# Kernel optimization log

Hardware: AMD Instinct MI355X
Metric: run time of the kernel (lower is better)

Reference implementation:

```python
import jax, jax.numpy as jnp
import numpy as np
from jax import lax

B, T, H, IN = 2048, 2048, 25, 1


def setup_inputs() -> dict:
    key = jax.random.key(0)
    ks = jax.random.split(key, 7)
    s = 1.0 / np.sqrt(H)  # PyTorch LSTM init scale
    return {
        "x": jax.random.normal(ks[0], (B, T, IN), dtype=jnp.float32),
        "w_ih": jax.random.uniform(ks[1], (4 * H, IN), jnp.float32, -s, s),
        "w_hh": jax.random.uniform(ks[2], (4 * H, H), jnp.float32, -s, s),
        "b_ih": jax.random.uniform(ks[3], (4 * H,), jnp.float32, -s, s),
        "b_hh": jax.random.uniform(ks[4], (4 * H,), jnp.float32, -s, s),
        "w_dense": jax.random.uniform(ks[5], (1, H), jnp.float32, -s, s),
        "b_dense": jax.random.uniform(ks[6], (1,), jnp.float32, -s, s),
    }


def reference(x, w_ih, w_hh, b_ih, b_hh, w_dense, b_dense):
    # x: [B, T, 1] -> scan over time on [T, B, *]
    xt = jnp.swapaxes(x, 0, 1)                     # [T, B, IN]
    x_proj = xt @ w_ih.T + (b_ih + b_hh)           # [T, B, 4H], input projection precomputed

    def step(carry, xp):
        h, c = carry
        gates = xp + h @ w_hh.T                    # [B, 4H]
        i, f, g, o = jnp.split(gates, 4, axis=-1)  # PyTorch gate order i,f,g,o
        i = jax.nn.sigmoid(i)
        f = jax.nn.sigmoid(f)
        g = jnp.tanh(g)
        o = jax.nn.sigmoid(o)
        c = f * c + i * g
        h = o * jnp.tanh(c)
        return (h, c), h

    h0 = jnp.zeros((x.shape[0], H), dtype=x.dtype)
    c0 = jnp.zeros((x.shape[0], H), dtype=x.dtype)
    _, hs = lax.scan(step, (h0, c0), x_proj)       # hs: [T, B, H]
    hs = jnp.swapaxes(hs, 0, 1)                    # [B, T, H]
    return hs @ w_dense.T + b_dense                # [B, T, 1]
```

## Files before the change

kernel.cpp:

```cpp
#include <hip/hip_runtime.h>

#define T_LEN 2048
#define HID   25
#define LOG2E 1.4426950408889634f

typedef float vf4 __attribute__((vector_size(16), may_alias));
typedef float vf2 __attribute__((vector_size(8),  may_alias));
typedef float f2  __attribute__((ext_vector_type(2)));

__device__ __forceinline__ float fast_rcp(float x) { return __builtin_amdgcn_rcpf(x); }
__device__ __forceinline__ float fast_exp2(float x) { return __builtin_amdgcn_exp2f(x); }


__global__ __attribute__((amdgpu_flat_work_group_size(256, 256),
                          amdgpu_waves_per_eu(1, 1)))
void lstm_fused(
    const float* __restrict__ x,
    const float* __restrict__ w_ih,
    const float* __restrict__ w_hh,
    const float* __restrict__ b_ih,
    const float* __restrict__ b_hh,
    const float* __restrict__ w_dense,
    const float* __restrict__ b_dense,
    float* __restrict__ out)
{
    const int tid  = threadIdx.x;
    const int u    = tid & 31;
    const int cb   = tid >> 5;
    const int b    = blockIdx.x * 8 + cb;
    const bool act = u < HID;

    __shared__ __align__(16) float hbuf[16][32];

    const float si = -LOG2E, sg = 2.f * LOG2E;

    f2 wI2[13], wF2[13], wG2[13], wO2[13];
#pragma unroll
    for (int m = 0; m < 12; ++m) {
        wI2[m] = act ? f2{si * w_hh[u * HID + m],             si * w_hh[u * HID + m + 12]}             : f2{0.f, 0.f};
        wF2[m] = act ? f2{si * w_hh[(HID + u) * HID + m],     si * w_hh[(HID + u) * HID + m + 12]}     : f2{0.f, 0.f};
        wG2[m] = act ? f2{sg * w_hh[(2 * HID + u) * HID + m], sg * w_hh[(2 * HID + u) * HID + m + 12]} : f2{0.f, 0.f};
        wO2[m] = act ? f2{si * w_hh[(3 * HID + u) * HID + m], si * w_hh[(3 * HID + u) * HID + m + 12]} : f2{0.f, 0.f};
    }
    wI2[12] = act ? f2{si * w_hh[u * HID + 24], 0.f}             : f2{0.f, 0.f};
    wF2[12] = act ? f2{si * w_hh[(HID + u) * HID + 24], 0.f}     : f2{0.f, 0.f};
    wG2[12] = act ? f2{sg * w_hh[(2 * HID + u) * HID + 24], 0.f} : f2{0.f, 0.f};
    wO2[12] = act ? f2{si * w_hh[(3 * HID + u) * HID + 24], 0.f} : f2{0.f, 0.f};

    const float bI  = act ? si * (b_ih[u] + b_hh[u]) : 0.f;
    const float bF  = act ? si * (b_ih[HID + u] + b_hh[HID + u]) : 0.f;
    const float bG  = act ? sg * (b_ih[2 * HID + u] + b_hh[2 * HID + u]) : 0.f;
    const float bO  = act ? si * (b_ih[3 * HID + u] + b_hh[3 * HID + u]) : 0.f;
    const float wxI = act ? si * w_ih[u] : 0.f;
    const float wxF = act ? si * w_ih[HID + u] : 0.f;
    const float wxG = act ? sg * w_ih[2 * HID + u] : 0.f;
    const float wxO = act ? si * w_ih[3 * HID + u] : 0.f;
    const float bd  = b_dense[0];

    f2 wd2[13];
#pragma unroll
    for (int m = 0; m < 12; ++m) wd2[m] = f2{w_dense[m], w_dense[m + 12]};
    wd2[12] = f2{w_dense[24], 0.f};

    hbuf[cb][u] = 0.f;
    hbuf[8 + cb][u] = 0.f;

    const int slot = (u < 12) ? 2 * u : (u < 24) ? 2 * u - 23 : 24;
    float* hwr = act ? &hbuf[cb][slot] : &hbuf[8 + cb][u];
    const vf4* r4 = (const vf4*)&hbuf[cb][0];
    const vf2* r2 = (const vf2*)&hbuf[cb][24];

    const float4* __restrict__ xp = (const float4*)(x + (size_t)b * T_LEN);
    float* __restrict__ orow = out + (size_t)b * T_LEN;

    f2 hp[13];
#pragma unroll
    for (int m = 0; m < 13; ++m) hp[m] = f2{0.f, 0.f};

    float c = 0.f;
    float yroll = 0.f;
    float4 xcur = xp[0];

    for (int it = 0; it < T_LEN / 4; ++it) {
        const int nx = (it + 1 < T_LEN / 4) ? it + 1 : it;
        float4 xnext = xp[nx];
        float xs[4] = {xcur.x, xcur.y, xcur.z, xcur.w};

#pragma unroll
        for (int s = 0; s < 4; ++s) {
            const float xv = xs[s];
            const int t = 4 * it + s;

            f2 accI = f2{fmaf(xv, wxI, bI), 0.f};
            f2 accF = f2{fmaf(xv, wxF, bF), 0.f};
            f2 accG = f2{fmaf(xv, wxG, bG), 0.f};
            f2 accO = f2{fmaf(xv, wxO, bO), 0.f};
#pragma unroll
            for (int m = 0; m < 13; ++m) {
                const f2 h = hp[m];
                accI = __builtin_elementwise_fma(h, wI2[m], accI);
                accF = __builtin_elementwise_fma(h, wF2[m], accF);
                accG = __builtin_elementwise_fma(h, wG2[m], accG);
                accO = __builtin_elementwise_fma(h, wO2[m], accO);
            }
            const float aI = accI.x + accI.y;
            const float aF = accF.x + accF.y;
            const float aG = accG.x + accG.y;
            const float aO = accO.x + accO.y;

            const float sI = fast_rcp(1.f + fast_exp2(aI));
            const float sF = fast_rcp(1.f + fast_exp2(aF));
            const float sO = fast_rcp(1.f + fast_exp2(aO));
            const float tG = fmaf(-2.f, fast_rcp(1.f + fast_exp2(aG)), 1.f);

            c = fmaf(sF, c, sI * tG);
            const float tC = fmaf(-2.f, fast_rcp(1.f + fast_exp2(2.f * LOG2E * c)), 1.f);
            const float hn = sO * tC;

            *hwr = hn;
            __asm__ __volatile__("" ::: "memory");
            {
                vf4 a0 = r4[0], a1 = r4[1], a2 = r4[2];
                vf4 a3 = r4[3], a4 = r4[4], a5 = r4[5];
                vf2 a6 = r2[0];
                hp[0]  = f2{a0[0], a0[1]}; hp[1]  = f2{a0[2], a0[3]};
                hp[2]  = f2{a1[0], a1[1]}; hp[3]  = f2{a1[2], a1[3]};
                hp[4]  = f2{a2[0], a2[1]}; hp[5]  = f2{a2[2], a2[3]};
                hp[6]  = f2{a3[0], a3[1]}; hp[7]  = f2{a3[2], a3[3]};
                hp[8]  = f2{a4[0], a4[1]}; hp[9]  = f2{a4[2], a4[3]};
                hp[10] = f2{a5[0], a5[1]}; hp[11] = f2{a5[2], a5[3]};
                hp[12] = f2{a6[0], a6[1]};
            }

            {
                f2 accY = f2{0.f, 0.f};
#pragma unroll
                for (int m = 0; m < 13; ++m)
                    accY = __builtin_elementwise_fma(hp[m], wd2[m], accY);
                const float ys = accY.x + accY.y;
                yroll = ((t & 31) == u) ? ys : yroll;
                if ((t & 31) == 31)
                    orow[(t & ~31) + u] = yroll + bd;
            }
        }
        xcur = xnext;
    }
}

extern "C" void kernel_launch(void* const* d_in, const int* in_sizes, int n_in,
                              void* d_out, int out_size, void* d_ws, size_t ws_size,
                              hipStream_t stream) {
    const float* x       = (const float*)d_in[0];
    const float* w_ih    = (const float*)d_in[1];
    const float* w_hh    = (const float*)d_in[2];
    const float* b_ih    = (const float*)d_in[3];
    const float* b_hh    = (const float*)d_in[4];
    const float* w_dense = (const float*)d_in[5];
    const float* b_dense = (const float*)d_in[6];
    float* out = (float*)d_out;

    lstm_fused<<<dim3(256), dim3(256), 0, stream>>>(x, w_ih, w_hh, b_ih, b_hh,
                                                    w_dense, b_dense, out);
}
```

Baseline: 592.1 us.

## Batch dense output projection over 32-step hidden-state history in LDS

Stores each timestep's hidden vector into a per-chain 32-row LDS history buffer instead of a single reused row. The per-step dense dot product and select are replaced by one projection every 32 steps, where each lane reads its own timestep row. The time loop is unrolled 32 deep with x prefetched eight float4 at a time, and a log2e scale is folded into the cell state. The cost is a larger LDS footprint, heavier unrolled code and more register pressure from the x prefetch arrays.

```diff
diff --git a/kernel.cpp b/kernel.cpp
--- a/kernel.cpp
+++ b/kernel.cpp
@@ -30,7 +30,7 @@
     const int b    = blockIdx.x * 8 + cb;
     const bool act = u < HID;
 
-    __shared__ __align__(16) float hbuf[16][32];
+    __shared__ __align__(16) float hist[8][32][36];
 
     const float si = -LOG2E, sg = 2.f * LOG2E;
 
@@ -62,13 +62,13 @@
     for (int m = 0; m < 12; ++m) wd2[m] = f2{w_dense[m], w_dense[m + 12]};
     wd2[12] = f2{w_dense[24], 0.f};
 
-    hbuf[cb][u] = 0.f;
-    hbuf[8 + cb][u] = 0.f;
+    hist[cb][u][25] = 0.f;
 
-    const int slot = (u < 12) ? 2 * u : (u < 24) ? 2 * u - 23 : 24;
-    float* hwr = act ? &hbuf[cb][slot] : &hbuf[8 + cb][u];
-    const vf4* r4 = (const vf4*)&hbuf[cb][0];
-    const vf2* r2 = (const vf2*)&hbuf[cb][24];
+    const int slot = act ? ((u < 12) ? 2 * u : (u < 24) ? 2 * u - 23 : 24)
+                         : (u + 1);
+    float* pw = &hist[cb][0][slot];
+    const float* pr = &hist[cb][0][0];
+    const float* py = &hist[cb][u][0];
 
     const float4* __restrict__ xp = (const float4*)(x + (size_t)b * T_LEN);
     float* __restrict__ orow = out + (size_t)b * T_LEN;
@@ -77,19 +77,23 @@
 #pragma unroll
     for (int m = 0; m < 13; ++m) hp[m] = f2{0.f, 0.f};
 
-    float c = 0.f;
-    float yroll = 0.f;
-    float4 xcur = xp[0];
+    float C = 0.f;
 
-    for (int it = 0; it < T_LEN / 4; ++it) {
-        const int nx = (it + 1 < T_LEN / 4) ? it + 1 : it;
-        float4 xnext = xp[nx];
-        float xs[4] = {xcur.x, xcur.y, xcur.z, xcur.w};
+    float4 xc[8];
+#pragma unroll
+    for (int i = 0; i < 8; ++i) xc[i] = xp[i];
+
+    for (int blk = 0; blk < 64; ++blk) {
+        const int nb = (blk < 63) ? blk + 1 : blk;
+        float4 xn[8];
+#pragma unroll
+        for (int i = 0; i < 8; ++i) xn[i] = xp[nb * 8 + i];
 
 #pragma unroll
-        for (int s = 0; s < 4; ++s) {
-            const float xv = xs[s];
-            const int t = 4 * it + s;
+        for (int j = 0; j < 32; ++j) {
+            const float4 xq = xc[j >> 2];
+            const float xv = ((j & 3) == 0) ? xq.x : ((j & 3) == 1) ? xq.y
+                           : ((j & 3) == 2) ? xq.z : xq.w;
 
             f2 accI = f2{fmaf(xv, wxI, bI), 0.f};
             f2 accF = f2{fmaf(xv, wxF, bF), 0.f};
@@ -111,18 +115,20 @@
             const float sI = fast_rcp(1.f + fast_exp2(aI));
             const float sF = fast_rcp(1.f + fast_exp2(aF));
             const float sO = fast_rcp(1.f + fast_exp2(aO));
-            const float tG = fmaf(-2.f, fast_rcp(1.f + fast_exp2(aG)), 1.f);
+            const float rG = fast_rcp(1.f + fast_exp2(aG));
+            const float tGs = fmaf(-4.f * LOG2E, rG, 2.f * LOG2E);
 
-            c = fmaf(sF, c, sI * tG);
-            const float tC = fmaf(-2.f, fast_rcp(1.f + fast_exp2(2.f * LOG2E * c)), 1.f);
+            C = fmaf(sF, C, sI * tGs);
+            const float tC = fmaf(-2.f, fast_rcp(1.f + fast_exp2(C)), 1.f);
             const float hn = sO * tC;
 
-            *hwr = hn;
+            pw[36 * j] = hn;
             __asm__ __volatile__("" ::: "memory");
             {
+                const vf4* r4 = (const vf4*)(pr + 36 * j);
                 vf4 a0 = r4[0], a1 = r4[1], a2 = r4[2];
                 vf4 a3 = r4[3], a4 = r4[4], a5 = r4[5];
-                vf2 a6 = r2[0];
+                vf2 a6 = *(const vf2*)(pr + 36 * j + 24);
                 hp[0]  = f2{a0[0], a0[1]}; hp[1]  = f2{a0[2], a0[3]};
                 hp[2]  = f2{a1[0], a1[1]}; hp[3]  = f2{a1[2], a1[3]};
                 hp[4]  = f2{a2[0], a2[1]}; hp[5]  = f2{a2[2], a2[3]};
@@ -132,18 +138,19 @@
                 hp[12] = f2{a6[0], a6[1]};
             }
 
-            {
+            if (j == 31) {
                 f2 accY = f2{0.f, 0.f};
 #pragma unroll
-                for (int m = 0; m < 13; ++m)
-                    accY = __builtin_elementwise_fma(hp[m], wd2[m], accY);
-                const float ys = accY.x + accY.y;
-                yroll = ((t & 31) == u) ? ys : yroll;
-                if ((t & 31) == 31)
-                    orow[(t & ~31) + u] = yroll + bd;
+                for (int m = 0; m < 13; ++m) {
+                    vf2 hm = ((const vf2*)py)[m];
+                    accY = __builtin_elementwise_fma(f2{hm[0], hm[1]}, wd2[m], accY);
+                }
+                orow[blk * 32 + u] = accY.x + accY.y + bd;
             }
         }
-        xcur = xnext;
+
+#pragma unroll
+        for (int i = 0; i < 8; ++i) xc[i] = xn[i];
     }
 }
 
```

New measurement: 580.7 us. About the same (-1.9%).
